# Kernel optimization log

Measured on AMD Instinct MI355X. Metric: run time of the kernel, lower is better.

The kernel has to match this reference:

```python
import jax, jax.numpy as jnp
import numpy as np

L, B, T, D, H = 8, 4, 1024, 1024, 16
DH = D // H
TPB, NB = 16, 64  # tokens_per_block, max_blocks; T == TPB*NB
EPS = 1e-5


def _block_causal_mask():
    idx = jnp.arange(T)
    causal = idx[:, None] >= idx[None, :]
    blk = idx // TPB
    block_diag = blk[:, None] == blk[None, :]
    return causal | block_diag  # [T, T] bool


def _ln(x, g, b):
    mu = jnp.mean(x, axis=-1, keepdims=True)
    var = jnp.mean(jnp.square(x - mu), axis=-1, keepdims=True)
    return (x - mu) * jax.lax.rsqrt(var + EPS) * g + b


def setup_inputs() -> dict:
    key = jax.random.key(0)
    ks = jax.random.split(key, 8)
    s = 0.02
    inp = {
        'sequences': jax.random.normal(ks[0], (B, T, D), jnp.float32),
        'Wq': jax.random.normal(ks[1], (L, D, D), jnp.float32) * s,
        'bq': jnp.zeros((L, D), jnp.float32),
        'Wk': jax.random.normal(ks[2], (L, D, D), jnp.float32) * s,
        'bk': jnp.zeros((L, D), jnp.float32),
        'Wv': jax.random.normal(ks[3], (L, D, D), jnp.float32) * s,
        'bv': jnp.zeros((L, D), jnp.float32),
        'Wp': jax.random.normal(ks[4], (L, D, D), jnp.float32) * s,
        'bp': jnp.zeros((L, D), jnp.float32),
        'ln1_g': jnp.ones((L, D), jnp.float32),
        'ln1_b': jnp.zeros((L, D), jnp.float32),
        'ln2_g': jnp.ones((L, D), jnp.float32),
        'ln2_b': jnp.zeros((L, D), jnp.float32),
        'W1': jax.random.normal(ks[5], (L, D, 4 * D), jnp.float32) * s,
        'b1': jnp.zeros((L, 4 * D), jnp.float32),
        'W2': jax.random.normal(ks[6], (L, 4 * D, D), jnp.float32) * s,
        'b2': jnp.zeros((L, D), jnp.float32),
        'lnf_g': jnp.ones((D,), jnp.float32),
        'lnf_b': jnp.zeros((D,), jnp.float32),
    }
    return inp


def reference(sequences, Wq, bq, Wk, bk, Wv, bv, Wp, bp,
              ln1_g, ln1_b, ln2_g, ln2_b, W1, b1, W2, b2, lnf_g, lnf_b):
    mask = _block_causal_mask()
    scale = 1.0 / np.sqrt(DH)
    x = sequences
    for i in range(L):
        h = _ln(x, ln1_g[i], ln1_b[i])
        q = (h @ Wq[i] + bq[i]).reshape(B, T, H, DH)
        k = (h @ Wk[i] + bk[i]).reshape(B, T, H, DH)
        v = (h @ Wv[i] + bv[i]).reshape(B, T, H, DH)
        att = jnp.einsum('bthd,bshd->bhts', q, k) * scale  # [B,H,T,T]
        att = jnp.where(mask, att, -jnp.inf)
        att = jax.nn.softmax(att, axis=-1)
        y = jnp.einsum('bhts,bshd->bthd', att, v).reshape(B, T, D)
        x = x + (y @ Wp[i] + bp[i])
        h2 = _ln(x, ln2_g[i], ln2_b[i])
        ff = jax.nn.gelu(h2 @ W1[i] + b1[i], approximate=False) @ W2[i] + b2[i]
        x = x + ff
    return _ln(x, lnf_g, lnf_b)
```

## Files before the change

kernel.cpp:

```cpp
#include <hip/hip_runtime.h>
#include <hip/hip_bf16.h>
#include <math.h>

#define B_ 4
#define T_ 1024
#define D_ 1024
#define H_ 16
#define DH_ 64
#define M_ 4096
#define QSTR_ 3072
#define EPS_ 1e-5f

typedef __attribute__((ext_vector_type(4))) float f32x4;
typedef __attribute__((ext_vector_type(8))) short s16x8;

#if __has_builtin(__builtin_amdgcn_exp2f)
#define EXP2F __builtin_amdgcn_exp2f
#else
#define EXP2F exp2f
#endif

__device__ __forceinline__ float gelu_f(float x) {
  return 0.5f * x * (1.0f + erff(x * 0.70710678118654752f));
}
__device__ __forceinline__ float b2f(unsigned short u) {
  union { unsigned int i; float f; } c; c.i = ((unsigned int)u) << 16; return c.f;
}
__device__ __forceinline__ unsigned short f2b(float f) {
  __hip_bfloat16 h = __float2bfloat16(f);
  return *reinterpret_cast<unsigned short*>(&h);
}
__device__ __forceinline__ void g2l16(void* l, const void* g) {
  __builtin_amdgcn_global_load_lds(
      (const __attribute__((address_space(1))) void*)g,
      (__attribute__((address_space(3))) void*)l, 16, 0, 0);
}

template<bool BF16OUT, bool ADDP>
__global__ __launch_bounds__(256) void ln_kernel(
    float* __restrict__ xio, const float* __restrict__ part,
    void* __restrict__ out,
    const float* __restrict__ g, const float* __restrict__ b) {
  const int row = blockIdx.x;
  const int tid = threadIdx.x;
  float* rp = xio + (size_t)row * D_;
  float4 v = *reinterpret_cast<const float4*>(rp + tid * 4);
  if (ADDP) {
    float4 pv = *reinterpret_cast<const float4*>(part + (size_t)row * D_ + tid * 4);
    v.x += pv.x; v.y += pv.y; v.z += pv.z; v.w += pv.w;
    *reinterpret_cast<float4*>(rp + tid * 4) = v;
  }
  float s = v.x + v.y + v.z + v.w;
  float s2 = v.x * v.x + v.y * v.y + v.z * v.z + v.w * v.w;
#pragma unroll
  for (int off = 1; off < 64; off <<= 1) {
    s += __shfl_xor(s, off);
    s2 += __shfl_xor(s2, off);
  }
  __shared__ float red[2][4];
  const int wid = tid >> 6;
  if ((tid & 63) == 0) { red[0][wid] = s; red[1][wid] = s2; }
  __syncthreads();
  s = red[0][0] + red[0][1] + red[0][2] + red[0][3];
  s2 = red[1][0] + red[1][1] + red[1][2] + red[1][3];
  const float mu = s * (1.0f / D_);
  const float var = s2 * (1.0f / D_) - mu * mu;
  const float rs = rsqrtf(var + EPS_);
  float4 gv = *reinterpret_cast<const float4*>(g + tid * 4);
  float4 bv = *reinterpret_cast<const float4*>(b + tid * 4);
  float o0 = (v.x - mu) * rs * gv.x + bv.x;
  float o1 = (v.y - mu) * rs * gv.y + bv.y;
  float o2 = (v.z - mu) * rs * gv.z + bv.z;
  float o3 = (v.w - mu) * rs * gv.w + bv.w;
  if (BF16OUT) {
    ushort4 pk;
    pk.x = f2b(o0); pk.y = f2b(o1); pk.z = f2b(o2); pk.w = f2b(o3);
    *reinterpret_cast<ushort4*>((unsigned short*)out + (size_t)row * D_ + tid * 4) = pk;
  } else {
    *reinterpret_cast<float4*>((float*)out + (size_t)row * D_ + tid * 4) =
        make_float4(o0, o1, o2, o3);
  }
}

__global__ __launch_bounds__(256) void concat_bias(
    const float* __restrict__ bq, const float* __restrict__ bk,
    const float* __restrict__ bv, float* __restrict__ out) {
  const int i = blockIdx.x * 256 + threadIdx.x;
  const int l = i / QSTR_, c = i % QSTR_;
  const float* src = (c < 1024) ? bq : ((c < 2048) ? bk : bv);
  out[i] = src[l * 1024 + (c & 1023)];
}

__device__ __forceinline__ void transpose_tile(
    const float* __restrict__ src, int sld,
    __hip_bfloat16* __restrict__ dst, int dld, int k0, int n0) {
  __shared__ float tile[32][33];
  const int t = threadIdx.x;
  const int r = t >> 3;
  const int cq = (t & 7) * 4;
  float4 vv = *reinterpret_cast<const float4*>(src + (size_t)(k0 + r) * sld + n0 + cq);
  tile[r][cq + 0] = vv.x; tile[r][cq + 1] = vv.y;
  tile[r][cq + 2] = vv.z; tile[r][cq + 3] = vv.w;
  __syncthreads();
  ushort4 o;
  o.x = f2b(tile[cq + 0][r]); o.y = f2b(tile[cq + 1][r]);
  o.z = f2b(tile[cq + 2][r]); o.w = f2b(tile[cq + 3][r]);
  *reinterpret_cast<ushort4*>((unsigned short*)dst + (size_t)(n0 + r) * dld + k0 + cq) = o;
}

struct TrAll {
  const float *wq, *wk, *wv, *wp, *w1, *w2;
  __hip_bfloat16 *dqkv, *dp, *d1, *d2;
};

__global__ __launch_bounds__(256) void transpose_all(TrAll a) {
  const int t = blockIdx.x;
  const float* src;
  __hip_bfloat16* dst;
  int sld, dld, k0, n0;
  if (t < 4096) {
    const int m = t >> 10, tile = t & 1023;
    k0 = (tile >> 5) * 32; n0 = (tile & 31) * 32;
    src = (m == 0) ? a.wq : (m == 1) ? a.wk : (m == 2) ? a.wv : a.wp;
    sld = 1024; dld = 1024;
    dst = (m < 3) ? (a.dqkv + (size_t)m * 1024 * 1024) : a.dp;
  } else if (t < 8192) {
    const int tile = t - 4096;
    k0 = (tile & 31) * 32; n0 = (tile >> 5) * 32;
    src = a.w1; sld = 4096; dst = a.d1; dld = 1024;
  } else {
    const int tile = t - 8192;
    k0 = (tile >> 5) * 32; n0 = (tile & 31) * 32;
    src = a.w2; sld = 1024; dst = a.d2; dld = 4096;
  }
  transpose_tile(src, sld, dst, dld, k0, n0);
}

template<int MODE, int BN>
__global__ __launch_bounds__(256) void gemm_mfma(
    const __hip_bfloat16* __restrict__ A,
    const __hip_bfloat16* __restrict__ Bt,
    const float* __restrict__ bias,
    void* __restrict__ Cout, int N, int K) {
  __shared__ short As[3][128 * 32];
  __shared__ short Bs[3][BN * 32];
  int bid = blockIdx.y * gridDim.x + blockIdx.x;
  const int nwg = gridDim.x * gridDim.y;
  bid = (bid & 7) * (nwg >> 3) + (bid >> 3);
  const int gn = (bid % gridDim.x) * BN;
  const int gm = (bid / gridDim.x) * 128;

  const int tid = threadIdx.x;
  const int wid = tid >> 6, lane = tid & 63;
  constexpr int MR = (BN == 128) ? 4 : 2;
  const int wm = (BN == 128) ? (wid >> 1) : wid;
  const int wn = (BN == 128) ? (wid & 1) : 0;
  const int fr = lane & 15, kg = lane >> 4;

  const int ldr = lane >> 2;
  const int ldk = (((lane & 3) ^ ((lane >> 3) & 3)) * 8);
  const unsigned short* ap =
      (const unsigned short*)A + (size_t)(gm + wid * 32 + ldr) * K + ldk;
  const unsigned short* bp =
      (const unsigned short*)Bt +
      (size_t)(gn + ((BN == 128) ? wid * 32 : wid * 16) + ldr) * K + ldk;

  const int nkt = K >> 5;

#define STAGE_T(t, buf)                                                    \
  {                                                                        \
    const unsigned short* a_ = ap + (size_t)(t) * 32;                      \
    g2l16((char*)As[buf] + (wid * 2) * 1024, a_);                          \
    g2l16((char*)As[buf] + (wid * 2 + 1) * 1024, a_ + (size_t)16 * K);     \
    const unsigned short* b_ = bp + (size_t)(t) * 32;                      \
    if (BN == 128) {                                                       \
      g2l16((char*)Bs[buf] + (wid * 2) * 1024, b_);                        \
      g2l16((char*)Bs[buf] + (wid * 2 + 1) * 1024, b_ + (size_t)16 * K);   \
    } else {                                                               \
      g2l16((char*)Bs[buf] + wid * 1024, b_);                              \
    }                                                                      \
  }

  STAGE_T(0, 0);
  STAGE_T(1, 1);

  const int cxa = (kg ^ ((fr >> 1) & 3)) * 8;
  f32x4 acc[MR][4] = {};
  for (int t = 0; t < nkt; ++t) {
    const int buf = t % 3;
    if (t + 2 < nkt) STAGE_T(t + 2, (t + 2) % 3);
    const int rem = nkt - 1 - t;
    if (rem >= 2) {
      if (BN == 128) asm volatile("s_waitcnt vmcnt(8)" ::: "memory");
      else           asm volatile("s_waitcnt vmcnt(6)" ::: "memory");
    } else if (rem == 1) {
      if (BN == 128) asm volatile("s_waitcnt vmcnt(4)" ::: "memory");
      else           asm volatile("s_waitcnt vmcnt(3)" ::: "memory");
    } else {
      asm volatile("s_waitcnt vmcnt(0)" ::: "memory");
    }
    __builtin_amdgcn_s_barrier();
    __builtin_amdgcn_sched_barrier(0);
    s16x8 af[MR], bfr[4];
#pragma unroll
    for (int m = 0; m < MR; ++m)
      af[m] = *reinterpret_cast<const s16x8*>(
          &As[buf][(wm * (16 * MR) + m * 16 + fr) * 32 + cxa]);
#pragma unroll
    for (int n = 0; n < 4; ++n)
      bfr[n] = *reinterpret_cast<const s16x8*>(
          &Bs[buf][(wn * 64 + n * 16 + fr) * 32 + cxa]);
#pragma unroll
    for (int m = 0; m < MR; ++m)
#pragma unroll
      for (int n = 0; n < 4; ++n)
        acc[m][n] = __builtin_amdgcn_mfma_f32_16x16x32_bf16(af[m], bfr[n], acc[m][n], 0, 0, 0);
    __builtin_amdgcn_sched_barrier(0);
    __builtin_amdgcn_s_barrier();
  }
#undef STAGE_T

  const int r0 = gm + wm * (16 * MR);
  const int c0 = gn + wn * 64;
  float bb[4];
#pragma unroll
  for (int n = 0; n < 4; ++n)
    bb[n] = bias ? bias[c0 + n * 16 + fr] : 0.0f;
#pragma unroll
  for (int m = 0; m < MR; ++m) {
#pragma unroll
    for (int j = 0; j < 4; ++j) {
      const int row = r0 + m * 16 + kg * 4 + j;
#pragma unroll
      for (int n = 0; n < 4; ++n) {
        float val = acc[m][n][j] + bb[n];
        const size_t idx = (size_t)row * N + c0 + n * 16 + fr;
        if (MODE == 0) {
          ((unsigned short*)Cout)[idx] = f2b(val);
        } else if (MODE == 1) {
          float* cp = (float*)Cout + idx;
          *cp = *cp + val;
        } else {
          ((unsigned short*)Cout)[idx] = f2b(gelu_f(val));
        }
      }
    }
  }
}

template<int MODE>
__global__ __launch_bounds__(512) void gemm_w256(
    const __hip_bfloat16* __restrict__ A,
    const __hip_bfloat16* __restrict__ Bt,
    const float* __restrict__ bias,
    void* __restrict__ Cout, float* __restrict__ P,
    int N, int K, int KS) {
  __shared__ short As[3][128 * 32];
  __shared__ short Bs[3][256 * 32];
  int bid = blockIdx.y * gridDim.x + blockIdx.x;
  const int nwg = gridDim.x * gridDim.y;
  bid = (bid & 7) * (nwg >> 3) + (bid >> 3);
  const int gn = (bid % gridDim.x) * 256;
  const int gm = (bid / gridDim.x) * 128;
  const int koff = (MODE == 3) ? blockIdx.z * KS : 0;

  const int tid = threadIdx.x;
  const int wid = tid >> 6, lane = tid & 63;
  const int wm = wid & 1, wn = wid >> 1;
  const int fr = lane & 15, kg = lane >> 4;

  const int ldr = lane >> 2;
  const int ldk = (((lane & 3) ^ ((lane >> 3) & 3)) * 8);
  const unsigned short* ap =
      (const unsigned short*)A + (size_t)(gm + wid * 16 + ldr) * K + koff + ldk;
  const unsigned short* bp =
      (const unsigned short*)Bt + (size_t)(gn + wid * 32 + ldr) * K + koff + ldk;

  const int nkt = ((MODE == 3) ? KS : K) >> 5;

#define STAGE_W(t, buf)                                                    \
  {                                                                        \
    g2l16((char*)As[buf] + wid * 1024, ap + (size_t)(t) * 32);             \
    const unsigned short* b_ = bp + (size_t)(t) * 32;                      \
    g2l16((char*)Bs[buf] + (wid * 2) * 1024, b_);                          \
    g2l16((char*)Bs[buf] + (wid * 2 + 1) * 1024, b_ + (size_t)16 * K);     \
  }

  STAGE_W(0, 0);
  STAGE_W(1, 1);

  const int cxa = (kg ^ ((fr >> 1) & 3)) * 8;
  f32x4 acc[4][4] = {};
  for (int t = 0; t < nkt; ++t) {
    const int buf = t % 3;
    if (t + 2 < nkt) STAGE_W(t + 2, (t + 2) % 3);
    const int rem = nkt - 1 - t;
    if (rem >= 2)      asm volatile("s_waitcnt vmcnt(6)" ::: "memory");
    else if (rem == 1) asm volatile("s_waitcnt vmcnt(3)" ::: "memory");
    else               asm volatile("s_waitcnt vmcnt(0)" ::: "memory");
    __builtin_amdgcn_s_barrier();
    __builtin_amdgcn_sched_barrier(0);
    s16x8 af[4], bfr[4];
#pragma unroll
    for (int m = 0; m < 4; ++m)
      af[m] = *reinterpret_cast<const s16x8*>(
          &As[buf][(wm * 64 + m * 16 + fr) * 32 + cxa]);
#pragma unroll
    for (int n = 0; n < 4; ++n)
      bfr[n] = *reinterpret_cast<const s16x8*>(
          &Bs[buf][(wn * 64 + n * 16 + fr) * 32 + cxa]);
#pragma unroll
    for (int m = 0; m < 4; ++m)
#pragma unroll
      for (int n = 0; n < 4; ++n)
        acc[m][n] = __builtin_amdgcn_mfma_f32_16x16x32_bf16(af[m], bfr[n], acc[m][n], 0, 0, 0);
    __builtin_amdgcn_sched_barrier(0);
    __builtin_amdgcn_s_barrier();
  }
#undef STAGE_W

  const int r0 = gm + wm * 64;
  const int c0 = gn + wn * 64;
  if (MODE == 3 && blockIdx.z == 1) {
#pragma unroll
    for (int m = 0; m < 4; ++m)
#pragma unroll
      for (int j = 0; j < 4; ++j) {
        const int row = r0 + m * 16 + kg * 4 + j;
#pragma unroll
        for (int n = 0; n < 4; ++n)
          P[(size_t)row * N + c0 + n * 16 + fr] = acc[m][n][j];
      }
    return;
  }
  float bb[4];
#pragma unroll
  for (int n = 0; n < 4; ++n)
    bb[n] = bias ? bias[c0 + n * 16 + fr] : 0.0f;
#pragma unroll
  for (int m = 0; m < 4; ++m) {
#pragma unroll
    for (int j = 0; j < 4; ++j) {
      const int row = r0 + m * 16 + kg * 4 + j;
#pragma unroll
      for (int n = 0; n < 4; ++n) {
        float val = acc[m][n][j] + bb[n];
        const size_t idx = (size_t)row * N + c0 + n * 16 + fr;
        if (MODE == 0) {
          ((unsigned short*)Cout)[idx] = f2b(val);
        } else if (MODE == 1 || MODE == 3) {
          float* cp = (float*)Cout + idx;
          *cp = *cp + val;
        } else {
          ((unsigned short*)Cout)[idx] = f2b(gelu_f(val));
        }
      }
    }
  }
}

__global__ __launch_bounds__(256) void attn_mfma(
    const __hip_bfloat16* __restrict__ qkv, __hip_bfloat16* __restrict__ yg) {
  const int qb = 7 - blockIdx.x;
  const int hh = blockIdx.y;
  const int bb = blockIdx.z;
  __shared__ short Qs[128 * 64];
  __shared__ short Ks[2][64 * 64];
  __shared__ short Vt[2][64 * 64];
  const int tid = threadIdx.x;
  const int wid = tid >> 6, lane = tid & 63;
  const int fr = lane & 15, kg = lane >> 4;
  const size_t qb_base = (size_t)bb * T_ * QSTR_ + (size_t)hh * DH_;
  const unsigned short* qgp = (const unsigned short*)qkv + qb_base;
  const unsigned short* kgp = qgp + 1024;
  const unsigned short* vgp = qgp + 2048;
  const float C = 0.125f * 1.4426950408889634f;

  const int r8 = lane >> 3, cp = lane & 7;
#pragma unroll
  for (int u = 0; u < 4; ++u) {
    const int row = wid * 32 + u * 8 + r8;
    const int c16 = cp ^ (row & 7);
    g2l16((char*)Qs + (wid * 32 + u * 8) * 128,
          qgp + (size_t)(qb * 128 + row) * QSTR_ + c16 * 8);
  }
#pragma unroll
  for (int u = 0; u < 2; ++u) {
    const int row = wid * 16 + u * 8 + r8;
    const int c16 = cp ^ (row & 7);
    g2l16((char*)Ks[0] + (wid * 16 + u * 8) * 128,
          kgp + (size_t)row * QSTR_ + c16 * 8);
  }
  const int kv0 = tid >> 3;
  const int d0 = (tid & 7) * 8;
  const int rot = tid & 7;
  s16x8 sva = *reinterpret_cast<const s16x8*>(vgp + (size_t)kv0 * QSTR_ + d0);
  s16x8 svb = *reinterpret_cast<const s16x8*>(vgp + (size_t)(32 + kv0) * QSTR_ + d0);

  asm volatile("s_waitcnt vmcnt(0)" ::: "memory");
  __syncthreads();
  s16x8 qf[2][2];
#pragma unroll
  for (int rg = 0; rg < 2; ++rg) {
    const int row = wid * 32 + rg * 16 + fr;
    const char* rp = (const char*)Qs + row * 128;
    qf[rg][0] = *reinterpret_cast<const s16x8*>(rp + (((0 + kg) ^ (row & 7)) << 4));
    qf[rg][1] = *reinterpret_cast<const s16x8*>(rp + (((4 + kg) ^ (row & 7)) << 4));
  }

  f32x4 acco[2][4] = {};
  float m_run[2][4], l_run[2][4];
#pragma unroll
  for (int rg = 0; rg < 2; ++rg)
#pragma unroll
    for (int j = 0; j < 4; ++j) { m_run[rg][j] = -INFINITY; l_run[rg][j] = 0.f; }

  const int q16hi = qb * 8 + wid * 2 + 1;
  const int ntile = 2 * qb + 2;
  for (int kt = 0; kt < ntile; ++kt) {
    const int buf = kt & 1;
    asm volatile("s_waitcnt vmcnt(0)" ::: "memory");
#pragma unroll
    for (int j = 0; j < 8; ++j) {
      const int jj = (j + rot) & 7;
      const int d = d0 + jj;
      *(short*)((char*)Vt[buf] + d * 128 + ((((kv0 >> 3) ^ jj) & 7) << 4) + (kv0 & 7) * 2) = sva[jj];
    }
#pragma unroll
    for (int j = 0; j < 8; ++j) {
      const int jj = (j + rot) & 7;
      const int d = d0 + jj;
      const int kv = 32 + kv0;
      *(short*)((char*)Vt[buf] + d * 128 + ((((kv >> 3) ^ jj) & 7) << 4) + (kv & 7) * 2) = svb[jj];
    }
    __syncthreads();
    if (kt + 1 < ntile) {
#pragma unroll
      for (int u = 0; u < 2; ++u) {
        const int row = wid * 16 + u * 8 + r8;
        const int c16 = cp ^ (row & 7);
        g2l16((char*)Ks[buf ^ 1] + (wid * 16 + u * 8) * 128,
              kgp + (size_t)((kt + 1) * 64 + row) * QSTR_ + c16 * 8);
      }
      sva = *reinterpret_cast<const s16x8*>(
          vgp + (size_t)((kt + 1) * 64 + kv0) * QSTR_ + d0);
      svb = *reinterpret_cast<const s16x8*>(
          vgp + (size_t)((kt + 1) * 64 + 32 + kv0) * QSTR_ + d0);
    }
    __builtin_amdgcn_sched_barrier(0);

    if (kt * 4 <= q16hi) {
      f32x4 accs[2][4] = {};
#pragma unroll
      for (int n = 0; n < 4; ++n) {
        const int row = n * 16 + fr;
        const char* rp = (const char*)Ks[buf] + row * 128;
        s16x8 kf0 = *reinterpret_cast<const s16x8*>(rp + (((0 + kg) ^ (row & 7)) << 4));
        s16x8 kf1 = *reinterpret_cast<const s16x8*>(rp + (((4 + kg) ^ (row & 7)) << 4));
#pragma unroll
        for (int rg = 0; rg < 2; ++rg) {
          accs[rg][n] = __builtin_amdgcn_mfma_f32_16x16x32_bf16(qf[rg][0], kf0, accs[rg][n], 0, 0, 0);
          accs[rg][n] = __builtin_amdgcn_mfma_f32_16x16x32_bf16(qf[rg][1], kf1, accs[rg][n], 0, 0, 0);
        }
      }
#pragma unroll
      for (int rg = 0; rg < 2; ++rg) {
        const int q16 = qb * 8 + wid * 2 + rg;
        float mloc[4] = {-3.0e38f, -3.0e38f, -3.0e38f, -3.0e38f};
#pragma unroll
        for (int n = 0; n < 4; ++n)
          if (kt * 4 + n <= q16)
#pragma unroll
            for (int j = 0; j < 4; ++j) mloc[j] = fmaxf(mloc[j], accs[rg][n][j]);
#pragma unroll
        for (int off = 1; off < 16; off <<= 1)
#pragma unroll
          for (int j = 0; j < 4; ++j) mloc[j] = fmaxf(mloc[j], __shfl_xor(mloc[j], off));
        float a_[4];
#pragma unroll
        for (int j = 0; j < 4; ++j) {
          const float mn = fmaxf(m_run[rg][j], mloc[j]);
          a_[j] = EXP2F((m_run[rg][j] - mn) * C);
          m_run[rg][j] = mn;
        }
        float psum[4] = {};
#pragma unroll
        for (int n = 0; n < 4; ++n) {
          const bool dead = (kt * 4 + n > q16);
          const int c16b = n * 2 + (fr >> 3);
#pragma unroll
          for (int j = 0; j < 4; ++j) {
            float p = dead ? 0.0f : EXP2F((accs[rg][n][j] - m_run[rg][j]) * C);
            psum[j] += p;
            const int row = wid * 32 + rg * 16 + kg * 4 + j;
            *(short*)((char*)Qs + row * 128 + (((c16b ^ (row & 7)) & 7) << 4) + (fr & 7) * 2) =
                (short)f2b(p);
          }
        }
#pragma unroll
        for (int j = 0; j < 4; ++j) l_run[rg][j] = l_run[rg][j] * a_[j] + psum[j];
#pragma unroll
        for (int dt = 0; dt < 4; ++dt)
#pragma unroll
          for (int j = 0; j < 4; ++j) acco[rg][dt][j] *= a_[j];
      }
#pragma unroll
      for (int rg = 0; rg < 2; ++rg) {
        const int prow = wid * 32 + rg * 16 + fr;
        const char* pp = (const char*)Qs + prow * 128;
#pragma unroll
        for (int kk = 0; kk < 2; ++kk) {
          const s16x8 pf = *reinterpret_cast<const s16x8*>(
              pp + ((((kk * 4 + kg) ^ (prow & 7)) & 7) << 4));
#pragma unroll
          for (int dt = 0; dt < 4; ++dt) {
            const int vrow = dt * 16 + fr;
            const s16x8 vf = *reinterpret_cast<const s16x8*>(
                (const char*)Vt[buf] + vrow * 128 + ((((kk * 4 + kg) ^ (vrow & 7)) & 7) << 4));
            acco[rg][dt] = __builtin_amdgcn_mfma_f32_16x16x32_bf16(pf, vf, acco[rg][dt], 0, 0, 0);
          }
        }
      }
    }
  }

#pragma unroll
  for (int off = 1; off < 16; off <<= 1)
#pragma unroll
    for (int rg = 0; rg < 2; ++rg)
#pragma unroll
      for (int j = 0; j < 4; ++j) l_run[rg][j] += __shfl_xor(l_run[rg][j], off);
  unsigned short* yp = (unsigned short*)yg + (size_t)bb * T_ * D_ + (size_t)hh * DH_;
#pragma unroll
  for (int rg = 0; rg < 2; ++rg) {
    float inv[4];
#pragma unroll
    for (int j = 0; j < 4; ++j) inv[j] = 1.0f / l_run[rg][j];
#pragma unroll
    for (int dt = 0; dt < 4; ++dt)
#pragma unroll
      for (int j = 0; j < 4; ++j) {
        const int row = qb * 128 + wid * 32 + rg * 16 + kg * 4 + j;
        yp[(size_t)row * D_ + dt * 16 + fr] = f2b(acco[rg][dt][j] * inv[j]);
      }
  }
}

extern "C" void kernel_launch(void* const* d_in, const int* in_sizes, int n_in,
                              void* d_out, int out_size, void* d_ws, size_t ws_size,
                              hipStream_t stream) {
  (void)in_sizes; (void)n_in; (void)out_size; (void)ws_size;
  const float* seq  = (const float*)d_in[0];
  const float* Wq   = (const float*)d_in[1];
  const float* bq   = (const float*)d_in[2];
  const float* Wk   = (const float*)d_in[3];
  const float* bk   = (const float*)d_in[4];
  const float* Wv   = (const float*)d_in[5];
  const float* bv   = (const float*)d_in[6];
  const float* Wp   = (const float*)d_in[7];
  const float* bp   = (const float*)d_in[8];
  const float* ln1g = (const float*)d_in[9];
  const float* ln1b = (const float*)d_in[10];
  const float* ln2g = (const float*)d_in[11];
  const float* ln2b = (const float*)d_in[12];
  const float* W1   = (const float*)d_in[13];
  const float* b1   = (const float*)d_in[14];
  const float* W2   = (const float*)d_in[15];
  const float* b2   = (const float*)d_in[16];
  const float* lnfg = (const float*)d_in[17];
  const float* lnfb = (const float*)d_in[18];

  float* x = (float*)d_out;
  char* ws = (char*)d_ws;
  const size_t MB = 1024ull * 1024ull;
  typedef __hip_bfloat16 bf16;
  bf16*  wtqkv = (bf16*)(ws + 0 * MB);
  bf16*  wtp   = (bf16*)(ws + 6 * MB);
  bf16*  wtF1  = (bf16*)(ws + 8 * MB);
  bf16*  wtF2  = (bf16*)(ws + 16 * MB);
  bf16*  hb    = (bf16*)(ws + 24 * MB);
  bf16*  qkv   = (bf16*)(ws + 32 * MB);
  bf16*  mid   = (bf16*)(ws + 56 * MB);
  float* bqkv  = (float*)(ws + 88 * MB);
  float* part  = (float*)(ws + 32 * MB);

  hipMemcpyAsync(x, seq, (size_t)M_ * D_ * sizeof(float), hipMemcpyDeviceToDevice, stream);

  const dim3 blk(256);
  const dim3 blkw(512);
  concat_bias<<<96, blk, 0, stream>>>(bq, bk, bv, bqkv);

  for (int i = 0; i < 8; ++i) {
    const size_t wo  = (size_t)i * D_ * D_;
    const size_t vo  = (size_t)i * D_;
    const size_t w1o = (size_t)i * D_ * 4 * D_;

    if (i == 0)
      ln_kernel<true, false><<<M_, blk, 0, stream>>>(x, nullptr, hb, ln1g + vo, ln1b + vo);
    else
      ln_kernel<true, true><<<M_, blk, 0, stream>>>(x, part, hb, ln1g + vo, ln1b + vo);
    TrAll ta;
    ta.wq = Wq + wo; ta.wk = Wk + wo; ta.wv = Wv + wo; ta.wp = Wp + wo;
    ta.w1 = W1 + w1o; ta.w2 = W2 + w1o;
    ta.dqkv = wtqkv; ta.dp = wtp; ta.d1 = wtF1; ta.d2 = wtF2;
    transpose_all<<<12288, blk, 0, stream>>>(ta);
    gemm_w256<0><<<dim3(12, 32), blkw, 0, stream>>>(
        hb, wtqkv, bqkv + (size_t)i * QSTR_, qkv, nullptr, QSTR_, 1024, 0);
    attn_mfma<<<dim3(8, 16, 4), blk, 0, stream>>>(qkv, hb);
    gemm_mfma<1, 64><<<dim3(16, 32), blk, 0, stream>>>(hb, wtp, bp + vo, x, 1024, 1024);
    ln_kernel<true, false><<<M_, blk, 0, stream>>>(x, nullptr, hb, ln2g + vo, ln2b + vo);
    gemm_w256<2><<<dim3(16, 32), blkw, 0, stream>>>(
        hb, wtF1, b1 + (size_t)i * 4096, mid, nullptr, 4096, 1024, 0);
    gemm_w256<3><<<dim3(4, 32, 2), blkw, 0, stream>>>(
        mid, wtF2, b2 + vo, x, part, 1024, 4096, 2048);
  }
  ln_kernel<false, true><<<M_, blk, 0, stream>>>(x, part, x, lnfg, lnfb);
}
```

Before: 2.180 ms.

## Split-K projection GEMM, 256x256 FFN1 tiles, and MFMA priority hints in attention

The output-projection GEMM now uses 128x128 tiles with a 2-way split-K. One half adds directly into x and the other writes a partial buffer, which the following LayerNorm folds in. The FFN1 GEMM moves to a 256x256 tile kernel with 8 waves for more operand reuse, at the cost of more registers and shared memory and a smaller grid of 256 blocks. The attention kernel wraps its MFMA sections in s_setprio to favour the matrix instructions. The partial buffer reuses the mid workspace, which is safe only because FFN1 overwrites it after the LayerNorm consumes it.

Measured after the change: 2.294 ms. 5.2% more time.

```diff
diff --git a/kernel.cpp b/kernel.cpp
--- a/kernel.cpp
+++ b/kernel.cpp
@@ -136,113 +136,188 @@
   transpose_tile(src, sld, dst, dld, k0, n0);
 }
 
-template<int MODE, int BN>
-__global__ __launch_bounds__(256) void gemm_mfma(
+__global__ __launch_bounds__(256) void gemm_skp(
     const __hip_bfloat16* __restrict__ A,
     const __hip_bfloat16* __restrict__ Bt,
     const float* __restrict__ bias,
-    void* __restrict__ Cout, int N, int K) {
+    float* __restrict__ X, float* __restrict__ P,
+    int N, int K, int KS) {
   __shared__ short As[3][128 * 32];
-  __shared__ short Bs[3][BN * 32];
+  __shared__ short Bs[3][128 * 32];
   int bid = blockIdx.y * gridDim.x + blockIdx.x;
   const int nwg = gridDim.x * gridDim.y;
   bid = (bid & 7) * (nwg >> 3) + (bid >> 3);
-  const int gn = (bid % gridDim.x) * BN;
+  const int gn = (bid % gridDim.x) * 128;
   const int gm = (bid / gridDim.x) * 128;
+  const int koff = blockIdx.z * KS;
 
   const int tid = threadIdx.x;
   const int wid = tid >> 6, lane = tid & 63;
-  constexpr int MR = (BN == 128) ? 4 : 2;
-  const int wm = (BN == 128) ? (wid >> 1) : wid;
-  const int wn = (BN == 128) ? (wid & 1) : 0;
+  const int wm = wid >> 1, wn = wid & 1;
   const int fr = lane & 15, kg = lane >> 4;
-
+  const int ldr = lane >> 2;
+  const int ldk = (((lane & 3) ^ ((lane >> 3) & 3)) * 8);
+  const unsigned short* ap =
+      (const unsigned short*)A + (size_t)(gm + wid * 32 + ldr) * K + koff + ldk;
+  const unsigned short* bp =
+      (const unsigned short*)Bt + (size_t)(gn + wid * 32 + ldr) * K + koff + ldk;
+  const int nkt = KS >> 5;
+
+#define STAGE_P(t, buf)                                                    \
+  {                                                                        \
+    const unsigned short* a_ = ap + (size_t)(t) * 32;                      \
+    g2l16((char*)As[buf] + (wid * 2) * 1024, a_);                          \
+    g2l16((char*)As[buf] + (wid * 2 + 1) * 1024, a_ + (size_t)16 * K);     \
+    const unsigned short* b_ = bp + (size_t)(t) * 32;                      \
+    g2l16((char*)Bs[buf] + (wid * 2) * 1024, b_);                          \
+    g2l16((char*)Bs[buf] + (wid * 2 + 1) * 1024, b_ + (size_t)16 * K);     \
+  }
+
+  STAGE_P(0, 0);
+  STAGE_P(1, 1);
+
+  const int cxa = (kg ^ ((fr >> 1) & 3)) * 8;
+  f32x4 acc[4][4] = {};
+  for (int t = 0; t < nkt; ++t) {
+    const int buf = t % 3;
+    if (t + 2 < nkt) STAGE_P(t + 2, (t + 2) % 3);
+    const int rem = nkt - 1 - t;
+    if (rem >= 2)      asm volatile("s_waitcnt vmcnt(8)" ::: "memory");
+    else if (rem == 1) asm volatile("s_waitcnt vmcnt(4)" ::: "memory");
+    else               asm volatile("s_waitcnt vmcnt(0)" ::: "memory");
+    __builtin_amdgcn_s_barrier();
+    __builtin_amdgcn_sched_barrier(0);
+    s16x8 af[4], bfr[4];
+#pragma unroll
+    for (int m = 0; m < 4; ++m)
+      af[m] = *reinterpret_cast<const s16x8*>(
+          &As[buf][(wm * 64 + m * 16 + fr) * 32 + cxa]);
+#pragma unroll
+    for (int n = 0; n < 4; ++n)
+      bfr[n] = *reinterpret_cast<const s16x8*>(
+          &Bs[buf][(wn * 64 + n * 16 + fr) * 32 + cxa]);
+#pragma unroll
+    for (int m = 0; m < 4; ++m)
+#pragma unroll
+      for (int n = 0; n < 4; ++n)
+        acc[m][n] = __builtin_amdgcn_mfma_f32_16x16x32_bf16(af[m], bfr[n], acc[m][n], 0, 0, 0);
+    __builtin_amdgcn_sched_barrier(0);
+    __builtin_amdgcn_s_barrier();
+  }
+#undef STAGE_P
+
+  const int r0 = gm + wm * 64;
+  const int c0 = gn + wn * 64;
+  if (blockIdx.z == 0) {
+    float bb[4];
+#pragma unroll
+    for (int n = 0; n < 4; ++n) bb[n] = bias[c0 + n * 16 + fr];
+#pragma unroll
+    for (int m = 0; m < 4; ++m)
+#pragma unroll
+      for (int j = 0; j < 4; ++j) {
+        const int row = r0 + m * 16 + kg * 4 + j;
+#pragma unroll
+        for (int n = 0; n < 4; ++n) {
+          const size_t idx = (size_t)row * N + c0 + n * 16 + fr;
+          X[idx] = X[idx] + acc[m][n][j] + bb[n];
+        }
+      }
+  } else {
+#pragma unroll
+    for (int m = 0; m < 4; ++m)
+#pragma unroll
+      for (int j = 0; j < 4; ++j) {
+        const int row = r0 + m * 16 + kg * 4 + j;
+#pragma unroll
+        for (int n = 0; n < 4; ++n)
+          P[(size_t)row * N + c0 + n * 16 + fr] = acc[m][n][j];
+      }
+  }
+}
+
+__global__ __launch_bounds__(512) void gemm_256(
+    const __hip_bfloat16* __restrict__ A,
+    const __hip_bfloat16* __restrict__ Bt,
+    const float* __restrict__ bias,
+    unsigned short* __restrict__ Cout, int N, int K) {
+  __shared__ short As[3][256 * 32];
+  __shared__ short Bs[3][256 * 32];
+  int bid = blockIdx.y * gridDim.x + blockIdx.x;
+  const int nwg = gridDim.x * gridDim.y;
+  bid = (bid & 7) * (nwg >> 3) + (bid >> 3);
+  const int gn = (bid % gridDim.x) * 256;
+  const int gm = (bid / gridDim.x) * 256;
+
+  const int tid = threadIdx.x;
+  const int wid = tid >> 6, lane = tid & 63;
+  const int wm = wid >> 2, wn = wid & 3;
+  const int fr = lane & 15, kg = lane >> 4;
   const int ldr = lane >> 2;
   const int ldk = (((lane & 3) ^ ((lane >> 3) & 3)) * 8);
   const unsigned short* ap =
       (const unsigned short*)A + (size_t)(gm + wid * 32 + ldr) * K + ldk;
   const unsigned short* bp =
-      (const unsigned short*)Bt +
-      (size_t)(gn + ((BN == 128) ? wid * 32 : wid * 16) + ldr) * K + ldk;
-
+      (const unsigned short*)Bt + (size_t)(gn + wid * 32 + ldr) * K + ldk;
   const int nkt = K >> 5;
 
-#define STAGE_T(t, buf)                                                    \
+#define STAGE_X(t, buf)                                                    \
   {                                                                        \
     const unsigned short* a_ = ap + (size_t)(t) * 32;                      \
     g2l16((char*)As[buf] + (wid * 2) * 1024, a_);                          \
     g2l16((char*)As[buf] + (wid * 2 + 1) * 1024, a_ + (size_t)16 * K);     \
     const unsigned short* b_ = bp + (size_t)(t) * 32;                      \
-    if (BN == 128) {                                                       \
-      g2l16((char*)Bs[buf] + (wid * 2) * 1024, b_);                        \
-      g2l16((char*)Bs[buf] + (wid * 2 + 1) * 1024, b_ + (size_t)16 * K);   \
-    } else {                                                               \
-      g2l16((char*)Bs[buf] + wid * 1024, b_);                              \
-    }                                                                      \
-  }
-
-  STAGE_T(0, 0);
-  STAGE_T(1, 1);
+    g2l16((char*)Bs[buf] + (wid * 2) * 1024, b_);                          \
+    g2l16((char*)Bs[buf] + (wid * 2 + 1) * 1024, b_ + (size_t)16 * K);     \
+  }
+
+  STAGE_X(0, 0);
+  STAGE_X(1, 1);
 
   const int cxa = (kg ^ ((fr >> 1) & 3)) * 8;
-  f32x4 acc[MR][4] = {};
+  f32x4 acc[8][4] = {};
   for (int t = 0; t < nkt; ++t) {
     const int buf = t % 3;
-    if (t + 2 < nkt) STAGE_T(t + 2, (t + 2) % 3);
+    if (t + 2 < nkt) STAGE_X(t + 2, (t + 2) % 3);
     const int rem = nkt - 1 - t;
-    if (rem >= 2) {
-      if (BN == 128) asm volatile("s_waitcnt vmcnt(8)" ::: "memory");
-      else           asm volatile("s_waitcnt vmcnt(6)" ::: "memory");
-    } else if (rem == 1) {
-      if (BN == 128) asm volatile("s_waitcnt vmcnt(4)" ::: "memory");
-      else           asm volatile("s_waitcnt vmcnt(3)" ::: "memory");
-    } else {
-      asm volatile("s_waitcnt vmcnt(0)" ::: "memory");
-    }
+    if (rem >= 2)      asm volatile("s_waitcnt vmcnt(8)" ::: "memory");
+    else if (rem == 1) asm volatile("s_waitcnt vmcnt(4)" ::: "memory");
+    else               asm volatile("s_waitcnt vmcnt(0)" ::: "memory");
     __builtin_amdgcn_s_barrier();
     __builtin_amdgcn_sched_barrier(0);
-    s16x8 af[MR], bfr[4];
-#pragma unroll
-    for (int m = 0; m < MR; ++m)
+    s16x8 af[8], bfr[4];
+#pragma unroll
+    for (int m = 0; m < 8; ++m)
       af[m] = *reinterpret_cast<const s16x8*>(
-          &As[buf][(wm * (16 * MR) + m * 16 + fr) * 32 + cxa]);
+          &As[buf][(wm * 128 + m * 16 + fr) * 32 + cxa]);
 #pragma unroll
     for (int n = 0; n < 4; ++n)
       bfr[n] = *reinterpret_cast<const s16x8*>(
           &Bs[buf][(wn * 64 + n * 16 + fr) * 32 + cxa]);
 #pragma unroll
-    for (int m = 0; m < MR; ++m)
+    for (int m = 0; m < 8; ++m)
 #pragma unroll
       for (int n = 0; n < 4; ++n)
         acc[m][n] = __builtin_amdgcn_mfma_f32_16x16x32_bf16(af[m], bfr[n], acc[m][n], 0, 0, 0);
     __builtin_amdgcn_sched_barrier(0);
     __builtin_amdgcn_s_barrier();
   }
-#undef STAGE_T
-
-  const int r0 = gm + wm * (16 * MR);
+#undef STAGE_X
+
+  const int r0 = gm + wm * 128;
   const int c0 = gn + wn * 64;
   float bb[4];
 #pragma unroll
-  for (int n = 0; n < 4; ++n)
-    bb[n] = bias ? bias[c0 + n * 16 + fr] : 0.0f;
-#pragma unroll
-  for (int m = 0; m < MR; ++m) {
+  for (int n = 0; n < 4; ++n) bb[n] = bias[c0 + n * 16 + fr];
+#pragma unroll
+  for (int m = 0; m < 8; ++m) {
 #pragma unroll
     for (int j = 0; j < 4; ++j) {
       const int row = r0 + m * 16 + kg * 4 + j;
 #pragma unroll
       for (int n = 0; n < 4; ++n) {
-        float val = acc[m][n][j] + bb[n];
-        const size_t idx = (size_t)row * N + c0 + n * 16 + fr;
-        if (MODE == 0) {
-          ((unsigned short*)Cout)[idx] = f2b(val);
-        } else if (MODE == 1) {
-          float* cp = (float*)Cout + idx;
-          *cp = *cp + val;
-        } else {
-          ((unsigned short*)Cout)[idx] = f2b(gelu_f(val));
-        }
+        const float val = acc[m][n][j] + bb[n];
+        Cout[(size_t)row * N + c0 + n * 16 + fr] = f2b(gelu_f(val));
       }
     }
   }
@@ -451,6 +526,7 @@
 
     if (kt * 4 <= q16hi) {
       f32x4 accs[2][4] = {};
+      __builtin_amdgcn_s_setprio(1);
 #pragma unroll
       for (int n = 0; n < 4; ++n) {
         const int row = n * 16 + fr;
@@ -463,6 +539,7 @@
           accs[rg][n] = __builtin_amdgcn_mfma_f32_16x16x32_bf16(qf[rg][1], kf1, accs[rg][n], 0, 0, 0);
         }
       }
+      __builtin_amdgcn_s_setprio(0);
 #pragma unroll
       for (int rg = 0; rg < 2; ++rg) {
         const int q16 = qb * 8 + wid * 2 + rg;
@@ -504,6 +581,7 @@
 #pragma unroll
           for (int j = 0; j < 4; ++j) acco[rg][dt][j] *= a_[j];
       }
+      __builtin_amdgcn_s_setprio(1);
 #pragma unroll
       for (int rg = 0; rg < 2; ++rg) {
         const int prow = wid * 32 + rg * 16 + fr;
@@ -521,6 +599,7 @@
           }
         }
       }
+      __builtin_amdgcn_s_setprio(0);
     }
   }
 
@@ -583,6 +662,7 @@
   bf16*  mid   = (bf16*)(ws + 56 * MB);
   float* bqkv  = (float*)(ws + 88 * MB);
   float* part  = (float*)(ws + 32 * MB);
+  float* part2 = (float*)(ws + 56 * MB);
 
   hipMemcpyAsync(x, seq, (size_t)M_ * D_ * sizeof(float), hipMemcpyDeviceToDevice, stream);
 
@@ -607,10 +687,11 @@
     gemm_w256<0><<<dim3(12, 32), blkw, 0, stream>>>(
         hb, wtqkv, bqkv + (size_t)i * QSTR_, qkv, nullptr, QSTR_, 1024, 0);
     attn_mfma<<<dim3(8, 16, 4), blk, 0, stream>>>(qkv, hb);
-    gemm_mfma<1, 64><<<dim3(16, 32), blk, 0, stream>>>(hb, wtp, bp + vo, x, 1024, 1024);
-    ln_kernel<true, false><<<M_, blk, 0, stream>>>(x, nullptr, hb, ln2g + vo, ln2b + vo);
-    gemm_w256<2><<<dim3(16, 32), blkw, 0, stream>>>(
-        hb, wtF1, b1 + (size_t)i * 4096, mid, nullptr, 4096, 1024, 0);
+    gemm_skp<<<dim3(8, 32, 2), blk, 0, stream>>>(
+        hb, wtp, bp + vo, x, part2, 1024, 1024, 512);
+    ln_kernel<true, true><<<M_, blk, 0, stream>>>(x, part2, hb, ln2g + vo, ln2b + vo);
+    gemm_256<<<dim3(16, 16), blkw, 0, stream>>>(
+        hb, wtF1, b1 + (size_t)i * 4096, (unsigned short*)mid, 4096, 1024);
     gemm_w256<3><<<dim3(4, 32, 2), blkw, 0, stream>>>(
         mid, wtF2, b2 + vo, x, part, 1024, 4096, 2048);
   }
```
